# Performance work log

Measured on AMD Instinct MI355X. Metric: run time of the kernel, lower is better.

Reference implementation:

```python
import jax, jax.numpy as jnp
import numpy as np

# Static model configuration (matches init_kwargs)
Hh, Ww = 48, 48
L = Hh * Ww            # 2304 flattened lattice sites
NH, HD = 8, 32         # heads, head_dim
D = NH * HD            # d_model = 256
MLP = 1024
NL = 4                 # num transformer blocks
RADIUS = 2             # local attention window radius
MAXD = 7               # relative position clipping
NB = 2 * MAXD + 1      # bias buckets per axis = 15
EPS = 1e-6
B = 4


def _coords():
    ys = jnp.arange(Hh)
    xs = jnp.arange(Ww)
    yy, xx = jnp.meshgrid(ys, xs, indexing='ij')
    return jnp.stack([yy, xx], axis=-1).reshape(L, 2)  # (L,2) int


def _local_mask():
    c = _coords()
    dy = jnp.abs(c[:, None, 0] - c[None, :, 0])
    dx = jnp.abs(c[:, None, 1] - c[None, :, 1])
    dy = jnp.minimum(dy, Hh - dy)  # periodic (torus)
    dx = jnp.minimum(dx, Ww - dx)
    allowed = (dy <= RADIUS) & (dx <= RADIUS)
    return jnp.where(allowed, 0.0, -1e9).astype(jnp.float32)  # (L,L)


def _rel_bias(rel_emb):
    c = _coords()
    dy = c[:, None, 0] - c[None, :, 0]
    dx = c[:, None, 1] - c[None, :, 1]
    # shortest signed periodic differences
    dy = (dy + Hh // 2) % Hh - Hh // 2
    dx = (dx + Ww // 2) % Ww - Ww // 2
    dyb = (jnp.clip(dy, -MAXD, MAXD) + MAXD).astype(jnp.int32)
    dxb = (jnp.clip(dx, -MAXD, MAXD) + MAXD).astype(jnp.int32)
    return rel_emb[:, dyb, dxb]  # (NH, L, L)


def _ln(x, s, b):
    mu = jnp.mean(x, axis=-1, keepdims=True)
    var = jnp.var(x, axis=-1, keepdims=True)
    return (x - mu) * jax.lax.rsqrt(var + EPS) * s + b


def setup_inputs() -> dict:
    key = jax.random.key(0)
    ks = jax.random.split(key, 16)
    sc = 0.05
    inp = {
        'x': jax.random.randint(ks[0], (B, Hh, Ww), 0, 2, dtype=jnp.int32),
        'Win': jax.random.normal(ks[1], (3, D), jnp.float32) * sc,
        'b_in': jnp.zeros((D,), jnp.float32),
        'lnA_s': jnp.ones((NL, D), jnp.float32),
        'lnA_b': jnp.zeros((NL, D), jnp.float32),
        'Wq': jax.random.normal(ks[2], (NL, D, NH, HD), jnp.float32) * sc,
        'bq': jnp.zeros((NL, NH, HD), jnp.float32),
        'Wk': jax.random.normal(ks[3], (NL, D, NH, HD), jnp.float32) * sc,
        'bk': jnp.zeros((NL, NH, HD), jnp.float32),
        'Wv': jax.random.normal(ks[4], (NL, D, NH, HD), jnp.float32) * sc,
        'bv': jnp.zeros((NL, NH, HD), jnp.float32),
        'Wo': jax.random.normal(ks[5], (NL, NH, HD, D), jnp.float32) * sc,
        'bo': jnp.zeros((NL, D), jnp.float32),
        'lnB_s': jnp.ones((NL, D), jnp.float32),
        'lnB_b': jnp.zeros((NL, D), jnp.float32),
        'W1': jax.random.normal(ks[6], (NL, D, MLP), jnp.float32) * sc,
        'b1': jnp.zeros((NL, MLP), jnp.float32),
        'W2': jax.random.normal(ks[7], (NL, MLP, D), jnp.float32) * sc,
        'b2': jnp.zeros((NL, D), jnp.float32),
        'rel_emb': jax.random.normal(ks[8], (NH, NB, NB), jnp.float32) * 0.02,
        'lnF_s': jnp.ones((D,), jnp.float32),
        'lnF_b': jnp.zeros((D,), jnp.float32),
        'Wout': jax.random.normal(ks[9], (D, 1), jnp.float32) * sc,
        'bout': jnp.zeros((1,), jnp.float32),
    }
    return inp


def reference(x, Win, b_in, lnA_s, lnA_b, Wq, bq, Wk, bk, Wv, bv, Wo, bo,
              lnB_s, lnB_b, W1, b1, W2, b2, rel_emb, lnF_s, lnF_b, Wout, bout):
    xf = x.astype(jnp.float32)[..., None]                     # (B,H,W,1)
    ys = jnp.arange(Hh, dtype=jnp.float32) / max(Hh - 1, 1)
    xs = jnp.arange(Ww, dtype=jnp.float32) / max(Ww - 1, 1)
    yy, xx = jnp.meshgrid(ys, xs, indexing='ij')
    coords = jnp.broadcast_to(jnp.stack([yy, xx], -1), (x.shape[0], Hh, Ww, 2))
    feats = jnp.concatenate([xf, coords], -1).reshape(x.shape[0], L, 3)

    h = feats @ Win + b_in                                    # (B,L,D)

    # combined additive attention bias: local periodic mask + learned 2D rel-pos bias
    cb = _local_mask()[None, None] + _rel_bias(rel_emb)[None]  # (1,NH,L,L)
    scale = 1.0 / np.sqrt(HD).astype(np.float32)

    for i in range(NL):
        y = _ln(h, lnA_s[i], lnA_b[i])
        q = jnp.einsum('bld,dhe->blhe', y, Wq[i]) + bq[i]
        k = jnp.einsum('bld,dhe->blhe', y, Wk[i]) + bk[i]
        v = jnp.einsum('bld,dhe->blhe', y, Wv[i]) + bv[i]
        scores = jnp.einsum('bqhe,bkhe->bhqk', q, k) * scale + cb
        p = jax.nn.softmax(scores, axis=-1)
        att = jnp.einsum('bhqk,bkhe->bqhe', p, v)
        y = jnp.einsum('bqhe,hed->bqd', att, Wo[i]) + bo[i]
        h = h + y
        y = _ln(h, lnB_s[i], lnB_b[i])
        y = jax.nn.gelu(y @ W1[i] + b1[i]) @ W2[i] + b2[i]
        h = h + y

    h = _ln(h, lnF_s, lnF_b)
    logits = (h @ Wout + bout)[..., 0].reshape(x.shape[0], Hh, Ww)
    return logits
```

## Files before the change

kernel.cpp:

```cpp
#include <hip/hip_runtime.h>
#include <hip/hip_bf16.h>
#include <math.h>

#define NT_   9216
#define D_    256
#define NH_   8
#define HD_   32
#define L_    2304
#define HH_   48
#define WW_   48
#define MLP_  1024
#define NL_   4

typedef __attribute__((ext_vector_type(8))) short bf16x8;
typedef __attribute__((ext_vector_type(4))) float f32x4;

__device__ __forceinline__ float gelu_tanh(float x) {
    const float c0 = 0.7978845608028654f;
    const float c1 = 0.044715f;
    float u = c0 * (x + c1 * x * x * x);
    return 0.5f * x * (1.0f + tanhf(u));
}

__device__ __forceinline__ void gload16(const void* gsrc, void* ldst) {
    __builtin_amdgcn_global_load_lds(
        (const __attribute__((address_space(1))) void*)gsrc,
        (__attribute__((address_space(3))) void*)ldst, 16, 0, 0);
}

__device__ __forceinline__ unsigned short f2bf(float f) {
    __hip_bfloat16 h = __float2bfloat16(f);
    return *(unsigned short*)&h;
}

__global__ void tcvt_kernel(const float* __restrict__ in, __hip_bfloat16* __restrict__ out,
                            int K, int N, int inLayerStride, int outLayerStride) {
    __shared__ float t[32][33];
    int l = blockIdx.z;
    int n0 = blockIdx.x * 32, k0 = blockIdx.y * 32;
    int tx = threadIdx.x, ty = threadIdx.y;
    const float* src = in + (size_t)l * inLayerStride;
    #pragma unroll
    for (int r = 0; r < 32; r += 8)
        t[ty + r][tx] = src[(size_t)(k0 + ty + r) * N + n0 + tx];
    __syncthreads();
    __hip_bfloat16* dst = out + (size_t)l * outLayerStride;
    #pragma unroll
    for (int r = 0; r < 32; r += 8)
        dst[(size_t)(n0 + ty + r) * K + k0 + tx] = __float2bfloat16(t[tx][ty + r]);
}

__global__ void bcat_kernel(const float* __restrict__ bq, const float* __restrict__ bk,
                            const float* __restrict__ bv, float* __restrict__ bqkv) {
    int l = blockIdx.x, n = threadIdx.x;
    float v = (n < 256) ? bq[l * 256 + n] : (n < 512 ? bk[l * 256 + n - 256] : bv[l * 256 + n - 512]);
    bqkv[l * 768 + n] = v;
}

__global__ void embed_kernel(const int* __restrict__ x, const float* __restrict__ Win,
                             const float* __restrict__ b_in, float* __restrict__ h) {
    int t = blockIdx.x, d = threadIdx.x;
    int l = t % L_;
    int yy = l / WW_, xx = l % WW_;
    float xv = (float)x[t];
    float yn = yy * (1.0f / 47.0f);
    float xn = xx * (1.0f / 47.0f);
    h[t * D_ + d] = xv * Win[d] + yn * Win[D_ + d] + xn * Win[2 * D_ + d] + b_in[d];
}

__global__ void ln_kernel(const float* __restrict__ h, const float* __restrict__ s,
                          const float* __restrict__ bb, __hip_bfloat16* __restrict__ y) {
    int wid = threadIdx.x >> 6, lane = threadIdx.x & 63;
    int t = (blockIdx.x << 2) + wid;
    float4 v = *(const float4*)(h + (size_t)t * D_ + lane * 4);
    float sum = v.x + v.y + v.z + v.w;
    float sq  = v.x * v.x + v.y * v.y + v.z * v.z + v.w * v.w;
    #pragma unroll
    for (int off = 32; off; off >>= 1) {
        sum += __shfl_xor(sum, off);
        sq  += __shfl_xor(sq,  off);
    }
    float mu  = sum * (1.0f / D_);
    float var = sq * (1.0f / D_) - mu * mu;
    float rs  = rsqrtf(var + 1e-6f);
    float4 s4 = *(const float4*)(s  + lane * 4);
    float4 b4 = *(const float4*)(bb + lane * 4);
    ushort4 o;
    o.x = f2bf((v.x - mu) * rs * s4.x + b4.x);
    o.y = f2bf((v.y - mu) * rs * s4.y + b4.y);
    o.z = f2bf((v.z - mu) * rs * s4.z + b4.z);
    o.w = f2bf((v.w - mu) * rs * s4.w + b4.w);
    *(ushort4*)(y + (size_t)t * D_ + lane * 4) = o;
}

__global__ void attn_kernel(const float* __restrict__ qkv, const float* __restrict__ rel_emb,
                            __hip_bfloat16* __restrict__ att) {
    const int t  = blockIdx.x;
    const int hh = threadIdx.x >> 5;
    const int j  = threadIdx.x & 31;
    const int b  = t / L_;
    const int l  = t - b * L_;
    const int yy = l / WW_, xx = l - yy * WW_;

    int oy2 = j / 5, ox2 = j - oy2 * 5;
    bool valid = (j < 25);
    int ny = yy + oy2 - 2; ny += (ny < 0) ? HH_ : 0; ny -= (ny >= HH_) ? HH_ : 0;
    int nx = xx + ox2 - 2; nx += (nx < 0) ? WW_ : 0; nx -= (nx >= WW_) ? WW_ : 0;
    int rowidx = valid ? (b * L_ + ny * WW_ + nx) : t;

    const float* qp = qkv + (size_t)t * 768 + hh * HD_;
    float4 q4[8];
    #pragma unroll
    for (int d = 0; d < 8; ++d) q4[d] = ((const float4*)qp)[d];

    const float* kp = qkv + (size_t)rowidx * 768 + 256 + hh * HD_;
    float dot = 0.f;
    #pragma unroll
    for (int d = 0; d < 8; ++d) {
        float4 k4 = ((const float4*)kp)[d];
        dot += q4[d].x * k4.x + q4[d].y * k4.y + q4[d].z * k4.z + q4[d].w * k4.w;
    }
    float bias = rel_emb[hh * 225 + (9 - oy2) * 15 + (9 - ox2)];
    float s = valid ? (dot * 0.17677669529663687f + bias) : -1e30f;

    float m = s;
    #pragma unroll
    for (int off = 16; off; off >>= 1) m = fmaxf(m, __shfl_xor(m, off, 32));
    float p = __expf(s - m);
    float sum = p;
    #pragma unroll
    for (int off = 16; off; off >>= 1) sum += __shfl_xor(sum, off, 32);
    float inv = 1.0f / sum;

    const float* vbase = qkv + 512 + hh * HD_ + j;
    float acc = 0.f;
    #pragma unroll
    for (int n = 0; n < 25; ++n) {
        float pn = __shfl(p, n, 32);
        int   rn = __shfl(rowidx, n, 32);
        acc += pn * vbase[(size_t)rn * 768];
    }
    att[t * D_ + hh * HD_ + j] = __float2bfloat16(acc * inv);
}

template<int EPI>
__global__ __launch_bounds__(256, 2)
void mgemm(const __hip_bfloat16* __restrict__ A, const __hip_bfloat16* __restrict__ BT,
           const float* __restrict__ bias, const float* res,
           float* Cf, __hip_bfloat16* Cb, int M, int N, int K) {
    __shared__ __hip_bfloat16 As[128 * 32];
    __shared__ __hip_bfloat16 Bs[128 * 32];
    const int bm = blockIdx.y * 128, bn = blockIdx.x * 128;
    const int tid = threadIdx.x, lane = tid & 63, wv = tid >> 6;
    const int wm = (wv >> 1) * 64, wn = (wv & 1) * 64;

    const __hip_bfloat16* aSrc = A + (size_t)(bm + 16 * wv + (lane >> 2)) * K + (lane & 3) * 8;
    const __hip_bfloat16* bSrc = BT + (size_t)(bn + 16 * wv + (lane >> 2)) * K + (lane & 3) * 8;
    __hip_bfloat16* aDst0 = As + wv * 512;
    __hip_bfloat16* aDst1 = As + (wv + 4) * 512;
    __hip_bfloat16* bDst0 = Bs + wv * 512;
    __hip_bfloat16* bDst1 = Bs + (wv + 4) * 512;
    const size_t rowJump = (size_t)64 * K;

    f32x4 acc[4][4];
    #pragma unroll
    for (int i = 0; i < 4; ++i)
        #pragma unroll
        for (int j = 0; j < 4; ++j)
            acc[i][j] = (f32x4){0.f, 0.f, 0.f, 0.f};

    const int rsel = (lane & 15);
    const int ko   = (lane >> 4) * 8;

    for (int k0 = 0; k0 < K; k0 += 32) {
        gload16(aSrc,            aDst0);
        gload16(aSrc + rowJump,  aDst1);
        gload16(bSrc,            bDst0);
        gload16(bSrc + rowJump,  bDst1);
        __syncthreads();

        bf16x8 af[4], bfr[4];
        #pragma unroll
        for (int f = 0; f < 4; ++f) {
            af[f]  = *(const bf16x8*)(As + (wm + f * 16 + rsel) * 32 + ko);
            bfr[f] = *(const bf16x8*)(Bs + (wn + f * 16 + rsel) * 32 + ko);
        }
        #pragma unroll
        for (int i = 0; i < 4; ++i)
            #pragma unroll
            for (int j = 0; j < 4; ++j)
                acc[i][j] = __builtin_amdgcn_mfma_f32_16x16x32_bf16(af[i], bfr[j], acc[i][j], 0, 0, 0);
        __syncthreads();
        aSrc += 32; bSrc += 32;
    }

    #pragma unroll
    for (int i = 0; i < 4; ++i) {
        #pragma unroll
        for (int r = 0; r < 4; ++r) {
            int rr = bm + wm + i * 16 + (lane >> 4) * 4 + r;
            #pragma unroll
            for (int j = 0; j < 4; ++j) {
                int cc = bn + wn + j * 16 + rsel;
                float v = acc[i][j][r] + bias[cc];
                if (EPI == 2) {
                    Cb[(size_t)rr * N + cc] = __float2bfloat16(gelu_tanh(v));
                } else {
                    if (EPI == 1) v += res[(size_t)rr * N + cc];
                    Cf[(size_t)rr * N + cc] = v;
                }
            }
        }
    }
}

__global__ void final_kernel(const float* __restrict__ h, const float* __restrict__ s,
                             const float* __restrict__ bb, const float* __restrict__ Wout,
                             const float* __restrict__ bout, float* __restrict__ out) {
    int t = blockIdx.x, d = threadIdx.x;
    float v = h[t * D_ + d];
    float a = v, b2 = v * v;
    #pragma unroll
    for (int off = 32; off; off >>= 1) {
        a  += __shfl_xor(a,  off);
        b2 += __shfl_xor(b2, off);
    }
    __shared__ float red[8];
    __shared__ float red2[4];
    int wave = threadIdx.x >> 6;
    if ((threadIdx.x & 63) == 0) { red[wave] = a; red[4 + wave] = b2; }
    __syncthreads();
    float sum   = red[0] + red[1] + red[2] + red[3];
    float sumsq = red[4] + red[5] + red[6] + red[7];
    float mu  = sum * (1.0f / D_);
    float var = sumsq * (1.0f / D_) - mu * mu;
    float rs  = rsqrtf(var + 1e-6f);
    float yv  = (v - mu) * rs * s[d] + bb[d];
    float p   = yv * Wout[d];
    #pragma unroll
    for (int off = 32; off; off >>= 1) p += __shfl_xor(p, off);
    if ((threadIdx.x & 63) == 0) red2[wave] = p;
    __syncthreads();
    if (threadIdx.x == 0)
        out[t] = red2[0] + red2[1] + red2[2] + red2[3] + bout[0];
}

extern "C" void kernel_launch(void* const* d_in, const int* in_sizes, int n_in,
                              void* d_out, int out_size, void* d_ws, size_t ws_size,
                              hipStream_t stream) {
    const int*   x       = (const int*)  d_in[0];
    const float* Win     = (const float*)d_in[1];
    const float* b_in    = (const float*)d_in[2];
    const float* lnA_s   = (const float*)d_in[3];
    const float* lnA_b   = (const float*)d_in[4];
    const float* Wq      = (const float*)d_in[5];
    const float* bq      = (const float*)d_in[6];
    const float* Wk      = (const float*)d_in[7];
    const float* bk      = (const float*)d_in[8];
    const float* Wv      = (const float*)d_in[9];
    const float* bv      = (const float*)d_in[10];
    const float* Wo      = (const float*)d_in[11];
    const float* bo      = (const float*)d_in[12];
    const float* lnB_s   = (const float*)d_in[13];
    const float* lnB_b   = (const float*)d_in[14];
    const float* W1      = (const float*)d_in[15];
    const float* b1      = (const float*)d_in[16];
    const float* W2      = (const float*)d_in[17];
    const float* b2      = (const float*)d_in[18];
    const float* rel_emb = (const float*)d_in[19];
    const float* lnF_s   = (const float*)d_in[20];
    const float* lnF_b   = (const float*)d_in[21];
    const float* Wout    = (const float*)d_in[22];
    const float* bout    = (const float*)d_in[23];
    float* out = (float*)d_out;

    float* ws = (float*)d_ws;
    float*          h      = ws;
    __hip_bfloat16* y      = (__hip_bfloat16*)(ws + 2359296);
    float*          qkv    = ws + 3538944;
    __hip_bfloat16* att    = (__hip_bfloat16*)(ws + 10616832);
    __hip_bfloat16* tbuf   = (__hip_bfloat16*)qkv;
    __hip_bfloat16* WqkvT  = (__hip_bfloat16*)(ws + 11796480);
    __hip_bfloat16* WoT    = WqkvT + 4 * 768 * 256;
    __hip_bfloat16* W1T    = WoT   + 4 * 256 * 256;
    __hip_bfloat16* W2T    = W1T   + 4 * 1024 * 256;
    float*          bqkv   = (float*)(W2T + 4 * 256 * 1024);

    dim3 blk(256);
    dim3 tb(32, 8);

    tcvt_kernel<<<dim3(8, 8, 4),  tb, 0, stream>>>(Wq, WqkvT,              256, 256,  65536, 196608);
    tcvt_kernel<<<dim3(8, 8, 4),  tb, 0, stream>>>(Wk, WqkvT + 256 * 256,  256, 256,  65536, 196608);
    tcvt_kernel<<<dim3(8, 8, 4),  tb, 0, stream>>>(Wv, WqkvT + 512 * 256,  256, 256,  65536, 196608);
    tcvt_kernel<<<dim3(8, 8, 4),  tb, 0, stream>>>(Wo, WoT,                256, 256,  65536, 65536);
    tcvt_kernel<<<dim3(32, 8, 4), tb, 0, stream>>>(W1, W1T,                256, 1024, 262144, 262144);
    tcvt_kernel<<<dim3(8, 32, 4), tb, 0, stream>>>(W2, W2T,                1024, 256, 262144, 262144);
    bcat_kernel<<<4, 768, 0, stream>>>(bq, bk, bv, bqkv);

    embed_kernel<<<NT_, blk, 0, stream>>>(x, Win, b_in, h);

    for (int l = 0; l < NL_; ++l) {
        const __hip_bfloat16* wqkv = WqkvT + (size_t)l * 768 * 256;
        const __hip_bfloat16* wo   = WoT   + (size_t)l * 256 * 256;
        const __hip_bfloat16* w1   = W1T   + (size_t)l * 1024 * 256;
        const __hip_bfloat16* w2   = W2T   + (size_t)l * 256 * 1024;

        ln_kernel<<<NT_ / 4, blk, 0, stream>>>(h, lnA_s + l * D_, lnA_b + l * D_, y);

        mgemm<0><<<dim3(6, 72), blk, 0, stream>>>(y, wqkv, bqkv + l * 768, nullptr,
                                                  qkv, nullptr, NT_, 768, 256);
        attn_kernel<<<NT_, blk, 0, stream>>>(qkv, rel_emb, att);
        mgemm<1><<<dim3(2, 72), blk, 0, stream>>>(att, wo, bo + l * D_, h,
                                                  h, nullptr, NT_, 256, 256);

        ln_kernel<<<NT_ / 4, blk, 0, stream>>>(h, lnB_s + l * D_, lnB_b + l * D_, y);

        mgemm<2><<<dim3(8, 72), blk, 0, stream>>>(y, w1, b1 + l * MLP_, nullptr,
                                                  nullptr, tbuf, NT_, 1024, 256);
        mgemm<1><<<dim3(2, 72), blk, 0, stream>>>(tbuf, w2, b2 + l * D_, h,
                                                  h, nullptr, NT_, 256, 1024);
    }

    final_kernel<<<NT_, blk, 0, stream>>>(h, lnF_s, lnF_b, Wout, bout, out);
}
```

Before: 747.9 us.

## Tile local attention into 8x8 spatial blocks with K/V halo in shared memory

```diff
diff --git a/kernel.cpp b/kernel.cpp
--- a/kernel.cpp
+++ b/kernel.cpp
@@ -93,54 +93,71 @@
     *(ushort4*)(y + (size_t)t * D_ + lane * 4) = o;
 }
 
-__global__ void attn_kernel(const float* __restrict__ qkv, const float* __restrict__ rel_emb,
-                            __hip_bfloat16* __restrict__ att) {
-    const int t  = blockIdx.x;
-    const int hh = threadIdx.x >> 5;
-    const int j  = threadIdx.x & 31;
-    const int b  = t / L_;
-    const int l  = t - b * L_;
-    const int yy = l / WW_, xx = l - yy * WW_;
-
-    int oy2 = j / 5, ox2 = j - oy2 * 5;
-    bool valid = (j < 25);
-    int ny = yy + oy2 - 2; ny += (ny < 0) ? HH_ : 0; ny -= (ny >= HH_) ? HH_ : 0;
-    int nx = xx + ox2 - 2; nx += (nx < 0) ? WW_ : 0; nx -= (nx >= WW_) ? WW_ : 0;
-    int rowidx = valid ? (b * L_ + ny * WW_ + nx) : t;
-
-    const float* qp = qkv + (size_t)t * 768 + hh * HD_;
-    float4 q4[8];
-    #pragma unroll
-    for (int d = 0; d < 8; ++d) q4[d] = ((const float4*)qp)[d];
-
-    const float* kp = qkv + (size_t)rowidx * 768 + 256 + hh * HD_;
-    float dot = 0.f;
-    #pragma unroll
-    for (int d = 0; d < 8; ++d) {
-        float4 k4 = ((const float4*)kp)[d];
-        dot += q4[d].x * k4.x + q4[d].y * k4.y + q4[d].z * k4.z + q4[d].w * k4.w;
-    }
-    float bias = rel_emb[hh * 225 + (9 - oy2) * 15 + (9 - ox2)];
-    float s = valid ? (dot * 0.17677669529663687f + bias) : -1e30f;
-
-    float m = s;
-    #pragma unroll
-    for (int off = 16; off; off >>= 1) m = fmaxf(m, __shfl_xor(m, off, 32));
-    float p = __expf(s - m);
-    float sum = p;
-    #pragma unroll
-    for (int off = 16; off; off >>= 1) sum += __shfl_xor(sum, off, 32);
-    float inv = 1.0f / sum;
-
-    const float* vbase = qkv + 512 + hh * HD_ + j;
-    float acc = 0.f;
-    #pragma unroll
-    for (int n = 0; n < 25; ++n) {
-        float pn = __shfl(p, n, 32);
-        int   rn = __shfl(rowidx, n, 32);
-        acc += pn * vbase[(size_t)rn * 768];
-    }
-    att[t * D_ + hh * HD_ + j] = __float2bfloat16(acc * inv);
+__global__ __launch_bounds__(256)
+void attn_kernel(const float* __restrict__ qkv, const float* __restrict__ rel_emb,
+                 __hip_bfloat16* __restrict__ att) {
+    __shared__ float ks[144 * 36];
+    __shared__ float vsd[144 * 36];
+
+    const int tile = blockIdx.x;
+    const int hh   = blockIdx.y;
+    const int b    = blockIdx.z;
+    const int ty   = tile / 6, tx = tile - ty * 6;
+    const int y0   = ty * 8,  x0  = tx * 8;
+    const int tid  = threadIdx.x;
+
+    for (int idx = tid; idx < 144 * 32; idx += 256) {
+        int r = idx >> 5, d = idx & 31;
+        int ly = r / 12, lx = r - ly * 12;
+        int gy = y0 + ly - 2; gy += (gy < 0) ? HH_ : 0; gy -= (gy >= HH_) ? HH_ : 0;
+        int gx = x0 + lx - 2; gx += (gx < 0) ? WW_ : 0; gx -= (gx >= WW_) ? WW_ : 0;
+        const float* row = qkv + (size_t)(b * L_ + gy * WW_ + gx) * 768 + hh * HD_;
+        ks[r * 36 + d]  = row[256 + d];
+        vsd[r * 36 + d] = row[512 + d];
+    }
+    __syncthreads();
+
+    const int g = tid >> 5;
+    const int j = tid & 31;
+    const bool valid = (j < 25);
+    const int oy2 = j / 5, ox2 = j - oy2 * 5;
+
+    const float bias = rel_emb[hh * 225 + (9 - oy2) * 15 + (9 - ox2)];
+
+    for (int s = 0; s < 8; ++s) {
+        const int t = b * L_ + (y0 + g) * WW_ + (x0 + s);
+
+        const float* qp = qkv + (size_t)t * 768 + hh * HD_;
+        const int hr = valid ? ((g + oy2) * 12 + (s + ox2)) : 0;
+        const float* kp = ks + hr * 36;
+
+        float dot = 0.f;
+        #pragma unroll
+        for (int d = 0; d < 8; ++d) {
+            float4 q4 = ((const float4*)qp)[d];
+            float4 k4 = ((const float4*)kp)[d];
+            dot += q4.x * k4.x + q4.y * k4.y + q4.z * k4.z + q4.w * k4.w;
+        }
+        float sc = valid ? (dot * 0.17677669529663687f + bias) : -1e30f;
+
+        float m = sc;
+        #pragma unroll
+        for (int off = 16; off; off >>= 1) m = fmaxf(m, __shfl_xor(m, off, 32));
+        float p = __expf(sc - m);
+        float sum = p;
+        #pragma unroll
+        for (int off = 16; off; off >>= 1) sum += __shfl_xor(sum, off, 32);
+        float inv = 1.0f / sum;
+
+        float acc = 0.f;
+        #pragma unroll
+        for (int n = 0; n < 25; ++n) {
+            float pn = __shfl(p, n, 32);
+            int   rn = (g + n / 5) * 12 + (s + n % 5);
+            acc += pn * vsd[rn * 36 + j];
+        }
+        att[t * D_ + hh * HD_ + j] = __float2bfloat16(acc * inv);
+    }
 }
 
 template<int EPI>
@@ -309,7 +326,7 @@
 
         mgemm<0><<<dim3(6, 72), blk, 0, stream>>>(y, wqkv, bqkv + l * 768, nullptr,
                                                   qkv, nullptr, NT_, 768, 256);
-        attn_kernel<<<NT_, blk, 0, stream>>>(qkv, rel_emb, att);
+        attn_kernel<<<dim3(36, 8, 4), blk, 0, stream>>>(qkv, rel_emb, att);
         mgemm<1><<<dim3(2, 72), blk, 0, stream>>>(att, wo, bo + l * D_, h,
                                                   h, nullptr, NT_, 256, 256);
 
```

Result: faster. 666.0 us (-10.9%).
